# Kernel tuning notes

Measured on AMD Instinct MI355X. Metric: run time of the kernel, lower is better.

The kernel has to match this reference:

```python
import jax, jax.numpy as jnp
import numpy as np

BS, H, S, D = 2, 16, 2048, 64  # bs, n_heads, seq_len (=q_len), head_dim
HEAD_SCALE = D ** (-0.5)


def setup_inputs() -> dict:
    key = jax.random.key(0)
    kq, kk, kv, kp = jax.random.split(key, 4)
    return {
        "q": jax.random.normal(kq, (BS, H, S, D), dtype=jnp.float32),
        "k": jax.random.normal(kk, (BS, H, D, S), dtype=jnp.float32),  # pre-transposed K
        "v": jax.random.normal(kv, (BS, H, S, D), dtype=jnp.float32),
        "prev": jax.random.normal(kp, (BS, H, S, S), dtype=jnp.float32),
        "scale": jnp.asarray(HEAD_SCALE, dtype=jnp.float32),
    }


def reference(q, k, v, prev, scale):
    # attn_scores = (q @ k) * scale + prev   [bs, h, q_len, seq_len]
    attn_scores = jnp.einsum("bhqd,bhds->bhqs", q, k) * scale + prev
    attn_weights = jax.nn.softmax(attn_scores, axis=-1)  # dropout p=0 -> identity
    output = jnp.einsum("bhqs,bhsd->bhqd", attn_weights, v)
    # res_attention=True -> return (output, attn_weights, attn_scores)
    return output, attn_weights, attn_scores
```

## Files before the change

### kernel.cpp

```cpp
#include <hip/hip_runtime.h>
#include <math.h>

#define S_LEN 2048
#define D_HEAD 64
#define BH 32
#define ROWS 16

typedef __attribute__((ext_vector_type(8))) short short8;
typedef __attribute__((ext_vector_type(4))) short short4v;
typedef __attribute__((ext_vector_type(4))) float f32x4;

#define SPAD 2052

__device__ __forceinline__ short f2bf(float f) {
  union { float f; unsigned u; } a; a.f = f;
  unsigned u = a.u;
  unsigned r = (u + 0x7fffu + ((u >> 16) & 1u)) >> 16;
  return (short)r;
}
__device__ __forceinline__ float bf2f(unsigned short h) {
  union { unsigned u; float f; } a; a.u = ((unsigned)h) << 16; return a.f;
}
__device__ __forceinline__ f32x4 ntl4(const float* p) { return __builtin_nontemporal_load((const f32x4*)p); }
__device__ __forceinline__ void  nts4(float* p, f32x4 v) { __builtin_nontemporal_store(v, (f32x4*)p); }

__global__ __launch_bounds__(256) void transpose_kernel(
    const float* __restrict__ kin, const float* __restrict__ vin,
    unsigned short* __restrict__ kT, unsigned short* __restrict__ vT)
{
  __shared__ float tile[64][65];
  const int bh = blockIdx.y;
  const int bx = blockIdx.x;
  const int t  = threadIdx.x;

  if (blockIdx.z == 0) {
    const float* in = kin + (size_t)bh * D_HEAD * S_LEN;
    #pragma unroll
    for (int p = 0; p < 4; ++p) {
      const int row = p * 16 + (t >> 4);
      f32x4 f = ntl4(in + (size_t)row * S_LEN + bx * 64 + (t & 15) * 4);
      tile[row][(t & 15) * 4 + 0] = f.x; tile[row][(t & 15) * 4 + 1] = f.y;
      tile[row][(t & 15) * 4 + 2] = f.z; tile[row][(t & 15) * 4 + 3] = f.w;
    }
    __syncthreads();
    union { unsigned short h[16]; uint4 q[2]; } u;
    #pragma unroll
    for (int i = 0; i < 16; ++i) u.h[i] = (unsigned short)f2bf(tile[(t & 3) * 16 + i][t >> 2]);
    uint4* dst = (uint4*)(kT + (size_t)bh * S_LEN * D_HEAD
                             + (size_t)(bx * 64 + (t >> 2)) * D_HEAD + (t & 3) * 16);
    dst[0] = u.q[0]; dst[1] = u.q[1];
  } else {
    const float* in = vin + (size_t)bh * S_LEN * D_HEAD;
    #pragma unroll
    for (int p = 0; p < 4; ++p) {
      const int row = p * 16 + (t >> 4);
      f32x4 f = ntl4(in + (size_t)(bx * 64 + row) * D_HEAD + (t & 15) * 4);
      tile[row][(t & 15) * 4 + 0] = f.x; tile[row][(t & 15) * 4 + 1] = f.y;
      tile[row][(t & 15) * 4 + 2] = f.z; tile[row][(t & 15) * 4 + 3] = f.w;
    }
    __syncthreads();
    union { unsigned short h[16]; uint4 q[2]; } u;
    #pragma unroll
    for (int i = 0; i < 16; ++i) u.h[i] = (unsigned short)f2bf(tile[(t & 3) * 16 + i][t >> 2]);
    uint4* dst = (uint4*)(vT + (size_t)bh * D_HEAD * S_LEN
                             + (size_t)(t >> 2) * S_LEN + bx * 64 + (t & 3) * 16);
    dst[0] = u.q[0]; dst[1] = u.q[1];
  }
}

__global__ __launch_bounds__(256, 2) void fused_kernel(
    const float* __restrict__ q, const unsigned short* __restrict__ kT,
    const float* __restrict__ prev, const float* __restrict__ scale_p,
    const unsigned short* __restrict__ vT,
    float* __restrict__ scores, float* __restrict__ weights, float* __restrict__ outO)
{
  __shared__ union {
    unsigned short s[ROWS][SPAD];
    float om[4][ROWS][68];
  } sh;
  __shared__ float rlv[ROWS];

  const int bh   = blockIdx.y;
  const int m0   = blockIdx.x * ROWS;
  const int tid  = threadIdx.x;
  const int w    = tid >> 6;
  const int lane = tid & 63;
  const int lr   = lane & 15;
  const int lg   = lane >> 4;
  const float scale = scale_p[0];

  const int row = tid >> 4;
  const int cq  = (tid & 15) * 4;
  const size_t rowoff = (size_t)bh * S_LEN * S_LEN + (size_t)(m0 + row) * S_LEN;
  const float* prevrow = prev + rowoff;

  f32x4 pf[16];
  #pragma unroll
  for (int u = 0; u < 16; ++u) pf[u] = ntl4(prevrow + cq + u * 64);

  short8 aq[2];
  {
    const float* qrow = q + ((size_t)bh * S_LEN + m0 + lr) * D_HEAD;
    #pragma unroll
    for (int kk = 0; kk < 2; ++kk) {
      f32x4 f0 = *(const f32x4*)(qrow + kk * 32 + lg * 8);
      f32x4 f1 = *(const f32x4*)(qrow + kk * 32 + lg * 8 + 4);
      short8 a;
      a[0]=f2bf(f0.x); a[1]=f2bf(f0.y); a[2]=f2bf(f0.z); a[3]=f2bf(f0.w);
      a[4]=f2bf(f1.x); a[5]=f2bf(f1.y); a[6]=f2bf(f1.z); a[7]=f2bf(f1.w);
      aq[kk] = a;
    }
  }

  const unsigned short* kbase = kT + (size_t)bh * S_LEN * D_HEAD;

  #pragma unroll 2
  for (int t8 = 0; t8 < 8; ++t8) {
    const int n0 = w * 512 + t8 * 64;
    f32x4 acc[4];
    #pragma unroll
    for (int nt = 0; nt < 4; ++nt) acc[nt] = (f32x4){0.f, 0.f, 0.f, 0.f};

    #pragma unroll
    for (int kk = 0; kk < 2; ++kk) {
      #pragma unroll
      for (int nt = 0; nt < 4; ++nt) {
        const short8 b = *(const short8*)(
            kbase + (size_t)(n0 + nt * 16 + lr) * D_HEAD + kk * 32 + lg * 8);
        acc[nt] = __builtin_amdgcn_mfma_f32_16x16x32_bf16(aq[kk], b, acc[nt], 0, 0, 0);
      }
    }
    #pragma unroll
    for (int nt = 0; nt < 4; ++nt)
      #pragma unroll
      for (int rg = 0; rg < 4; ++rg)
        sh.s[lg * 4 + rg][n0 + nt * 16 + lr] = (unsigned short)f2bf(acc[nt][rg]);
  }
  __syncthreads();

  float* srow = scores + rowoff;
  float sum = 0.f;
  #pragma unroll
  for (int u = 0; u < 32; ++u) {
    const int c = cq + u * 64;
    const f32x4 p = pf[u & 15];
    if (u < 16) pf[u & 15] = ntl4(prevrow + cq + (u + 16) * 64);
    short4v h = *(const short4v*)&sh.s[row][c];
    f32x4 s;
    s.x = bf2f((unsigned short)h[0]) * scale + p.x;
    s.y = bf2f((unsigned short)h[1]) * scale + p.y;
    s.z = bf2f((unsigned short)h[2]) * scale + p.z;
    s.w = bf2f((unsigned short)h[3]) * scale + p.w;
    nts4(srow + c, s);
    const float e0 = __expf(s.x), e1 = __expf(s.y), e2 = __expf(s.z), e3 = __expf(s.w);
    sum += (e0 + e1) + (e2 + e3);
    short4v g;
    g[0] = f2bf(e0); g[1] = f2bf(e1); g[2] = f2bf(e2); g[3] = f2bf(e3);
    *(short4v*)&sh.s[row][c] = g;
  }

  #pragma unroll
  for (int msk = 1; msk <= 8; msk <<= 1)
    sum += __shfl_xor(sum, msk, 64);
  const float rl = 1.0f / sum;
  if ((tid & 15) == 0) rlv[row] = rl;
  __syncthreads();

  const unsigned short* vbase = vT + (size_t)bh * D_HEAD * S_LEN;
  float* wrow = weights + rowoff;
  f32x4 accp[4];
  #pragma unroll
  for (int ct = 0; ct < 4; ++ct) accp[ct] = (f32x4){0.f, 0.f, 0.f, 0.f};

  #pragma unroll 2
  for (int i = 0; i < 16; ++i) {
    const int c4 = w * 512 + i * 32 + lg * 8;
    short4v h0 = *(const short4v*)&sh.s[lr][c4];
    short4v h1 = *(const short4v*)&sh.s[lr][c4 + 4];
    short8 a;
    a[0]=h0[0]; a[1]=h0[1]; a[2]=h0[2]; a[3]=h0[3];
    a[4]=h1[0]; a[5]=h1[1]; a[6]=h1[2]; a[7]=h1[3];
    #pragma unroll
    for (int ct = 0; ct < 4; ++ct) {
      const short8 b = *(const short8*)(vbase + (size_t)(ct * 16 + lr) * S_LEN + c4);
      accp[ct] = __builtin_amdgcn_mfma_f32_16x16x32_bf16(a, b, accp[ct], 0, 0, 0);
    }
    const int cA = cq + i * 64;
    const int cB = cA + 1024;
    short4v wA = *(const short4v*)&sh.s[row][cA];
    short4v wB = *(const short4v*)&sh.s[row][cB];
    f32x4 eA, eB;
    eA.x = bf2f((unsigned short)wA[0]) * rl;
    eA.y = bf2f((unsigned short)wA[1]) * rl;
    eA.z = bf2f((unsigned short)wA[2]) * rl;
    eA.w = bf2f((unsigned short)wA[3]) * rl;
    eB.x = bf2f((unsigned short)wB[0]) * rl;
    eB.y = bf2f((unsigned short)wB[1]) * rl;
    eB.z = bf2f((unsigned short)wB[2]) * rl;
    eB.w = bf2f((unsigned short)wB[3]) * rl;
    nts4(wrow + cA, eA);
    nts4(wrow + cB, eB);
  }
  __syncthreads();

  #pragma unroll
  for (int ct = 0; ct < 4; ++ct)
    #pragma unroll
    for (int rg = 0; rg < 4; ++rg)
      sh.om[w][lg * 4 + rg][ct * 16 + lr] = accp[ct][rg];
  __syncthreads();

  {
    const int d4 = (tid & 15) * 4;
    const float rls = rlv[row];
    f32x4 v;
    #pragma unroll
    for (int i = 0; i < 4; ++i)
      v[i] = (sh.om[0][row][d4 + i] + sh.om[1][row][d4 + i]
            + sh.om[2][row][d4 + i] + sh.om[3][row][d4 + i]) * rls;
    nts4(outO + ((size_t)bh * S_LEN + m0 + row) * D_HEAD + d4, v);
  }
}

extern "C" void kernel_launch(void* const* d_in, const int* in_sizes, int n_in,
                              void* d_out, int out_size, void* d_ws, size_t ws_size,
                              hipStream_t stream)
{
  const float* q     = (const float*)d_in[0];
  const float* kin   = (const float*)d_in[1];
  const float* vin   = (const float*)d_in[2];
  const float* prev  = (const float*)d_in[3];
  const float* scale = (const float*)d_in[4];

  float* O  = (float*)d_out;
  float* W  = O + (size_t)BH * S_LEN * D_HEAD;
  float* Sc = W + (size_t)BH * S_LEN * S_LEN;

  unsigned short* kT = (unsigned short*)d_ws;
  unsigned short* vT = kT + (size_t)BH * S_LEN * D_HEAD;

  dim3 tgrid(S_LEN / 64, BH, 2);
  hipLaunchKernelGGL(transpose_kernel, tgrid, dim3(256), 0, stream, kin, vin, kT, vT);

  dim3 grid(S_LEN / ROWS, BH);
  hipLaunchKernelGGL(fused_kernel, grid, dim3(256), 0, stream,
                     q, kT, prev, scale, vT, Sc, W, O);
}
```

Measured before the change: 418.8 us.

## Interleave QK, softmax and PV phases across column halves in fused attention

Splits the 2048 score columns into two halves and software-pipelines the phases. The second half's QK^T MFMA tiles are issued during the first half's scale/add/exp pass, and the first half's P·V MFMAs run during the second half's exp pass. The remaining P·V MFMAs are interleaved with the normalized weight stores. The aim is to hide MFMA and LDS latency behind the bandwidth-bound prev/score/weight traffic and to drop one barrier plus the shared reciprocal array, at the cost of more register pressure and a more intricate schedule.

```diff
diff --git a/kernel.cpp b/kernel.cpp
--- a/kernel.cpp
+++ b/kernel.cpp
@@ -78,7 +78,6 @@
     unsigned short s[ROWS][SPAD];
     float om[4][ROWS][68];
   } sh;
-  __shared__ float rlv[ROWS];
 
   const int bh   = blockIdx.y;
   const int m0   = blockIdx.x * ROWS;
@@ -113,14 +112,13 @@
   }
 
   const unsigned short* kbase = kT + (size_t)bh * S_LEN * D_HEAD;
-
-  #pragma unroll 2
-  for (int t8 = 0; t8 < 8; ++t8) {
-    const int n0 = w * 512 + t8 * 64;
+  const unsigned short* vbase = vT + (size_t)bh * D_HEAD * S_LEN;
+  float* srow = scores + rowoff;
+
+  auto p1_tile = [&](int n0) {
     f32x4 acc[4];
     #pragma unroll
     for (int nt = 0; nt < 4; ++nt) acc[nt] = (f32x4){0.f, 0.f, 0.f, 0.f};
-
     #pragma unroll
     for (int kk = 0; kk < 2; ++kk) {
       #pragma unroll
@@ -135,16 +133,28 @@
       #pragma unroll
       for (int rg = 0; rg < 4; ++rg)
         sh.s[lg * 4 + rg][n0 + nt * 16 + lr] = (unsigned short)f2bf(acc[nt][rg]);
-  }
-  __syncthreads();
-
-  float* srow = scores + rowoff;
+  };
+
+  f32x4 accp[4];
+  #pragma unroll
+  for (int ct = 0; ct < 4; ++ct) accp[ct] = (f32x4){0.f, 0.f, 0.f, 0.f};
+
+  auto pv_iter = [&](int c4) {
+    short4v h0 = *(const short4v*)&sh.s[lr][c4];
+    short4v h1 = *(const short4v*)&sh.s[lr][c4 + 4];
+    short8 a;
+    a[0]=h0[0]; a[1]=h0[1]; a[2]=h0[2]; a[3]=h0[3];
+    a[4]=h1[0]; a[5]=h1[1]; a[6]=h1[2]; a[7]=h1[3];
+    #pragma unroll
+    for (int ct = 0; ct < 4; ++ct) {
+      const short8 b = *(const short8*)(vbase + (size_t)(ct * 16 + lr) * S_LEN + c4);
+      accp[ct] = __builtin_amdgcn_mfma_f32_16x16x32_bf16(a, b, accp[ct], 0, 0, 0);
+    }
+  };
+
   float sum = 0.f;
-  #pragma unroll
-  for (int u = 0; u < 32; ++u) {
-    const int c = cq + u * 64;
-    const f32x4 p = pf[u & 15];
-    if (u < 16) pf[u & 15] = ntl4(prevrow + cq + (u + 16) * 64);
+
+  auto p2_chunk = [&](int c, f32x4 p) {
     short4v h = *(const short4v*)&sh.s[row][c];
     f32x4 s;
     s.x = bf2f((unsigned short)h[0]) * scale + p.x;
@@ -157,49 +167,48 @@
     short4v g;
     g[0] = f2bf(e0); g[1] = f2bf(e1); g[2] = f2bf(e2); g[3] = f2bf(e3);
     *(short4v*)&sh.s[row][c] = g;
+  };
+
+  #pragma unroll
+  for (int t8 = 0; t8 < 4; ++t8) p1_tile(w * 256 + t8 * 64);
+  __syncthreads();
+
+  #pragma unroll
+  for (int u = 0; u < 16; ++u) {
+    const f32x4 p = pf[u];
+    pf[u] = ntl4(prevrow + 1024 + cq + u * 64);
+    p2_chunk(cq + u * 64, p);
+    if ((u & 3) == 3) p1_tile(1024 + w * 256 + (u >> 2) * 64);
+  }
+  __syncthreads();
+
+  #pragma unroll
+  for (int u = 0; u < 16; ++u) {
+    p2_chunk(1024 + cq + u * 64, pf[u]);
+    if (u & 1) pv_iter(w * 256 + (u >> 1) * 32 + lg * 8);
   }
 
   #pragma unroll
   for (int msk = 1; msk <= 8; msk <<= 1)
     sum += __shfl_xor(sum, msk, 64);
   const float rl = 1.0f / sum;
-  if ((tid & 15) == 0) rlv[row] = rl;
-  __syncthreads();
-
-  const unsigned short* vbase = vT + (size_t)bh * D_HEAD * S_LEN;
+  __syncthreads();
+
   float* wrow = weights + rowoff;
-  f32x4 accp[4];
-  #pragma unroll
-  for (int ct = 0; ct < 4; ++ct) accp[ct] = (f32x4){0.f, 0.f, 0.f, 0.f};
-
-  #pragma unroll 2
-  for (int i = 0; i < 16; ++i) {
-    const int c4 = w * 512 + i * 32 + lg * 8;
-    short4v h0 = *(const short4v*)&sh.s[lr][c4];
-    short4v h1 = *(const short4v*)&sh.s[lr][c4 + 4];
-    short8 a;
-    a[0]=h0[0]; a[1]=h0[1]; a[2]=h0[2]; a[3]=h0[3];
-    a[4]=h1[0]; a[5]=h1[1]; a[6]=h1[2]; a[7]=h1[3];
-    #pragma unroll
-    for (int ct = 0; ct < 4; ++ct) {
-      const short8 b = *(const short8*)(vbase + (size_t)(ct * 16 + lr) * S_LEN + c4);
-      accp[ct] = __builtin_amdgcn_mfma_f32_16x16x32_bf16(a, b, accp[ct], 0, 0, 0);
-    }
-    const int cA = cq + i * 64;
-    const int cB = cA + 1024;
-    short4v wA = *(const short4v*)&sh.s[row][cA];
-    short4v wB = *(const short4v*)&sh.s[row][cB];
-    f32x4 eA, eB;
-    eA.x = bf2f((unsigned short)wA[0]) * rl;
-    eA.y = bf2f((unsigned short)wA[1]) * rl;
-    eA.z = bf2f((unsigned short)wA[2]) * rl;
-    eA.w = bf2f((unsigned short)wA[3]) * rl;
-    eB.x = bf2f((unsigned short)wB[0]) * rl;
-    eB.y = bf2f((unsigned short)wB[1]) * rl;
-    eB.z = bf2f((unsigned short)wB[2]) * rl;
-    eB.w = bf2f((unsigned short)wB[3]) * rl;
-    nts4(wrow + cA, eA);
-    nts4(wrow + cB, eB);
+  #pragma unroll
+  for (int i = 0; i < 8; ++i) {
+    pv_iter(1024 + w * 256 + i * 32 + lg * 8);
+    #pragma unroll
+    for (int v = 0; v < 4; ++v) {
+      const int c = cq + (i * 4 + v) * 64;
+      short4v hw = *(const short4v*)&sh.s[row][c];
+      f32x4 e;
+      e.x = bf2f((unsigned short)hw[0]) * rl;
+      e.y = bf2f((unsigned short)hw[1]) * rl;
+      e.z = bf2f((unsigned short)hw[2]) * rl;
+      e.w = bf2f((unsigned short)hw[3]) * rl;
+      nts4(wrow + c, e);
+    }
   }
   __syncthreads();
 
@@ -212,12 +221,11 @@
 
   {
     const int d4 = (tid & 15) * 4;
-    const float rls = rlv[row];
     f32x4 v;
     #pragma unroll
     for (int i = 0; i < 4; ++i)
       v[i] = (sh.om[0][row][d4 + i] + sh.om[1][row][d4 + i]
-            + sh.om[2][row][d4 + i] + sh.om[3][row][d4 + i]) * rls;
+            + sh.om[2][row][d4 + i] + sh.om[3][row][d4 + i]) * rl;
     nts4(outO + ((size_t)bh * S_LEN + m0 + row) * D_HEAD + d4, v);
   }
 }
```

After: 452.1 us. 1.08x slower.

## Remap softmax pass to wave-owned columns and drop barrier before exp pass

Applied to the files above, without the earlier changes.

Each wave now handles the score/exp pass over its own 512-column slice, the same columns it just produced with MFMA. That lets the block-wide barrier between the QK MFMA and the softmax pass go away. Row sums become per-wave partials, reduced through a small shared array after the PV MFMA loop, and the weight writes move after the PV loop and a barrier. The cost is a second sweep over shared memory for the weights and per-row stores with narrower 64-column spans per wave.

```diff
diff --git a/kernel.cpp b/kernel.cpp
--- a/kernel.cpp
+++ b/kernel.cpp
@@ -78,7 +78,7 @@
     unsigned short s[ROWS][SPAD];
     float om[4][ROWS][68];
   } sh;
-  __shared__ float rlv[ROWS];
+  __shared__ float lred[4][ROWS];
 
   const int bh   = blockIdx.y;
   const int m0   = blockIdx.x * ROWS;
@@ -89,14 +89,15 @@
   const int lg   = lane >> 4;
   const float scale = scale_p[0];
 
-  const int row = tid >> 4;
-  const int cq  = (tid & 15) * 4;
-  const size_t rowoff = (size_t)bh * S_LEN * S_LEN + (size_t)(m0 + row) * S_LEN;
-  const float* prevrow = prev + rowoff;
+  const int coff = w * 512 + lr * 4;
+  const float* pbase = prev    + (size_t)bh * S_LEN * S_LEN + (size_t)m0 * S_LEN + coff;
+  float*       sbase = scores  + (size_t)bh * S_LEN * S_LEN + (size_t)m0 * S_LEN + coff;
+  float*       wbase = weights + (size_t)bh * S_LEN * S_LEN + (size_t)m0 * S_LEN + coff;
 
   f32x4 pf[16];
   #pragma unroll
-  for (int u = 0; u < 16; ++u) pf[u] = ntl4(prevrow + cq + u * 64);
+  for (int j = 0; j < 16; ++j)
+    pf[j] = ntl4(pbase + (size_t)((j >> 3) * 4 + lg) * S_LEN + (j & 7) * 64);
 
   short8 aq[2];
   {
@@ -113,6 +114,7 @@
   }
 
   const unsigned short* kbase = kT + (size_t)bh * S_LEN * D_HEAD;
+  const unsigned short* vbase = vT + (size_t)bh * D_HEAD * S_LEN;
 
   #pragma unroll 2
   for (int t8 = 0; t8 < 8; ++t8) {
@@ -136,38 +138,40 @@
       for (int rg = 0; rg < 4; ++rg)
         sh.s[lg * 4 + rg][n0 + nt * 16 + lr] = (unsigned short)f2bf(acc[nt][rg]);
   }
-  __syncthreads();
-
-  float* srow = scores + rowoff;
-  float sum = 0.f;
-  #pragma unroll
-  for (int u = 0; u < 32; ++u) {
-    const int c = cq + u * 64;
-    const f32x4 p = pf[u & 15];
-    if (u < 16) pf[u & 15] = ntl4(prevrow + cq + (u + 16) * 64);
+
+  float sums[4] = {0.f, 0.f, 0.f, 0.f};
+  #pragma unroll
+  for (int j = 0; j < 32; ++j) {
+    const int it = j >> 3;
+    const int u  = j & 7;
+    const int row = it * 4 + lg;
+    const f32x4 p = pf[j & 15];
+    if (j < 16)
+      pf[j & 15] = ntl4(pbase + (size_t)(((j + 16) >> 3) * 4 + lg) * S_LEN + u * 64);
+    const int c = coff + u * 64;
     short4v h = *(const short4v*)&sh.s[row][c];
     f32x4 s;
     s.x = bf2f((unsigned short)h[0]) * scale + p.x;
     s.y = bf2f((unsigned short)h[1]) * scale + p.y;
     s.z = bf2f((unsigned short)h[2]) * scale + p.z;
     s.w = bf2f((unsigned short)h[3]) * scale + p.w;
-    nts4(srow + c, s);
+    nts4(sbase + (size_t)row * S_LEN + u * 64, s);
     const float e0 = __expf(s.x), e1 = __expf(s.y), e2 = __expf(s.z), e3 = __expf(s.w);
-    sum += (e0 + e1) + (e2 + e3);
+    sums[it] += (e0 + e1) + (e2 + e3);
     short4v g;
     g[0] = f2bf(e0); g[1] = f2bf(e1); g[2] = f2bf(e2); g[3] = f2bf(e3);
     *(short4v*)&sh.s[row][c] = g;
   }
 
   #pragma unroll
-  for (int msk = 1; msk <= 8; msk <<= 1)
-    sum += __shfl_xor(sum, msk, 64);
-  const float rl = 1.0f / sum;
-  if ((tid & 15) == 0) rlv[row] = rl;
-  __syncthreads();
-
-  const unsigned short* vbase = vT + (size_t)bh * D_HEAD * S_LEN;
-  float* wrow = weights + rowoff;
+  for (int it = 0; it < 4; ++it) {
+    float s2 = sums[it];
+    #pragma unroll
+    for (int msk = 1; msk <= 8; msk <<= 1)
+      s2 += __shfl_xor(s2, msk, 64);
+    if (lr == 0) lred[w][it * 4 + lg] = s2;
+  }
+
   f32x4 accp[4];
   #pragma unroll
   for (int ct = 0; ct < 4; ++ct) accp[ct] = (f32x4){0.f, 0.f, 0.f, 0.f};
@@ -185,21 +189,28 @@
       const short8 b = *(const short8*)(vbase + (size_t)(ct * 16 + lr) * S_LEN + c4);
       accp[ct] = __builtin_amdgcn_mfma_f32_16x16x32_bf16(a, b, accp[ct], 0, 0, 0);
     }
-    const int cA = cq + i * 64;
-    const int cB = cA + 1024;
-    short4v wA = *(const short4v*)&sh.s[row][cA];
-    short4v wB = *(const short4v*)&sh.s[row][cB];
-    f32x4 eA, eB;
-    eA.x = bf2f((unsigned short)wA[0]) * rl;
-    eA.y = bf2f((unsigned short)wA[1]) * rl;
-    eA.z = bf2f((unsigned short)wA[2]) * rl;
-    eA.w = bf2f((unsigned short)wA[3]) * rl;
-    eB.x = bf2f((unsigned short)wB[0]) * rl;
-    eB.y = bf2f((unsigned short)wB[1]) * rl;
-    eB.z = bf2f((unsigned short)wB[2]) * rl;
-    eB.w = bf2f((unsigned short)wB[3]) * rl;
-    nts4(wrow + cA, eA);
-    nts4(wrow + cB, eB);
+  }
+  __syncthreads();
+
+  float rl[4];
+  #pragma unroll
+  for (int it = 0; it < 4; ++it) {
+    const int row = it * 4 + lg;
+    rl[it] = 1.0f / (lred[0][row] + lred[1][row] + lred[2][row] + lred[3][row]);
+  }
+  #pragma unroll
+  for (int j = 0; j < 32; ++j) {
+    const int it = j >> 3;
+    const int u  = j & 7;
+    const int row = it * 4 + lg;
+    const int c = coff + u * 64;
+    short4v hw = *(const short4v*)&sh.s[row][c];
+    f32x4 e;
+    e.x = bf2f((unsigned short)hw[0]) * rl[it];
+    e.y = bf2f((unsigned short)hw[1]) * rl[it];
+    e.z = bf2f((unsigned short)hw[2]) * rl[it];
+    e.w = bf2f((unsigned short)hw[3]) * rl[it];
+    nts4(wbase + (size_t)row * S_LEN + u * 64, e);
   }
   __syncthreads();
 
@@ -211,8 +222,9 @@
   __syncthreads();
 
   {
-    const int d4 = (tid & 15) * 4;
-    const float rls = rlv[row];
+    const int row = tid >> 4;
+    const int d4  = (tid & 15) * 4;
+    const float rls = 1.0f / (lred[0][row] + lred[1][row] + lred[2][row] + lred[3][row]);
     f32x4 v;
     #pragma unroll
     for (int i = 0; i < 4; ++i)
```

After: 433.4 us. 3.5% more time.
